# Optimization experiments

Hardware: AMD Instinct MI355X
Metric: run time of the kernel (lower is better)

## Reference

```python
import jax, jax.numpy as jnp
import numpy as np

NUM_HEADS = 12
NUM_BN = 4
HIDDEN = 768
HEAD_DIM = HIDDEN // NUM_HEADS  # 64
SCALE = HEAD_DIM ** -0.5


def setup_inputs() -> dict:
    key = jax.random.key(0)
    k0, k1, k2, k3 = jax.random.split(key, 4)
    B, S = 8, 8192
    x = jax.random.normal(k0, (B, S, HIDDEN), dtype=jnp.float32)
    w_kv = jax.random.normal(k1, (2 * HIDDEN, HIDDEN), dtype=jnp.float32) * 0.02
    w_q = jax.random.normal(k2, (HIDDEN, HIDDEN), dtype=jnp.float32) * 0.02
    w_out = jax.random.normal(k3, (HIDDEN, HIDDEN), dtype=jnp.float32) * 0.02
    b_out = jnp.zeros((HIDDEN,), dtype=jnp.float32)
    return {"x": x, "w_kv": w_kv, "w_q": w_q, "w_out": w_out, "b_out": b_out}


def reference(x, w_kv, w_q, w_out, b_out):
    B, S, H = x.shape
    # kv projection over all tokens: [B, S, 2H] -> split (kv, heads, head_dim)
    kv = (x @ w_kv.T).reshape(B, S, 2, NUM_HEADS, HEAD_DIM)
    k = jnp.transpose(kv[:, :, 0], (0, 2, 1, 3))  # [B, h, S, d]
    v = jnp.transpose(kv[:, :, 1], (0, 2, 1, 3))  # [B, h, S, d]
    # q projection over first NUM_BN tokens only: [B, h, NUM_BN, d]
    q = (x[:, :NUM_BN] @ w_q.T).reshape(B, NUM_BN, NUM_HEADS, HEAD_DIM)
    q = jnp.transpose(q, (0, 2, 1, 3))
    # attention: [B, h, NUM_BN, S]
    att = jax.nn.softmax(jnp.einsum("bhxd,bhyd->bhxy", q, k) * SCALE, axis=-1)
    out = jnp.einsum("bhxy,bhyd->bhxd", att, v)  # [B, h, NUM_BN, d]
    out = jnp.transpose(out, (0, 2, 1, 3)).reshape(B, NUM_BN, H)
    return out @ w_out.T + b_out
```

## Files before the change

### kernel.cpp

```cpp
#include <hip/hip_runtime.h>

typedef unsigned short u16;
typedef __attribute__((ext_vector_type(8))) short short8;
typedef __attribute__((ext_vector_type(4))) float f32x4;
typedef __attribute__((ext_vector_type(8))) __bf16 bf16x8;

__device__ __forceinline__ float b2f(u16 u) {
  unsigned int i = ((unsigned int)u) << 16;
  return __builtin_bit_cast(float, i);
}
__device__ __forceinline__ u16 f2b(float f) {
  unsigned int i = __builtin_bit_cast(unsigned int, f);
  i += 0x7fffu + ((i >> 16) & 1u);
  return (u16)(i >> 16);
}

__global__ __launch_bounds__(256) void cvt_bf16(const float* __restrict__ in,
                                                u16* __restrict__ out, int n8) {
  int i = blockIdx.x * 256 + threadIdx.x;
  if (i >= n8) return;
  f32x4 v0 = *(const f32x4*)(in + (size_t)i * 8);
  f32x4 v1 = *(const f32x4*)(in + (size_t)i * 8 + 4);
  short8 o;
  o[0] = (short)f2b(v0.x); o[1] = (short)f2b(v0.y);
  o[2] = (short)f2b(v0.z); o[3] = (short)f2b(v0.w);
  o[4] = (short)f2b(v1.x); o[5] = (short)f2b(v1.y);
  o[6] = (short)f2b(v1.z); o[7] = (short)f2b(v1.w);
  *(short8*)(out + (size_t)i * 8) = o;
}

__global__ __launch_bounds__(256) void kv_gemm_mfma(const u16* __restrict__ A,
                                                    const u16* __restrict__ B,
                                                    u16* __restrict__ KV, int nb) {
  __shared__ u16 As[128 * 32];
  __shared__ u16 Bs[128 * 32];
  const int tid = threadIdx.x;
  const int lane = tid & 63;
  const int w = tid >> 6;
  const int wr = w >> 1, wc = w & 1;
  const int fr = lane & 15;
  const int fq = lane >> 4;

  const int bid0 = blockIdx.x;
  const int cpx = gridDim.x >> 3;
  const int bid = (bid0 & 7) * cpx + (bid0 >> 3);

  const int nt = bid % 12, mt = bid / 12;
  const int m0 = mt * 128, n0 = nt * 128;

  f32x4 accT[4][4] = {};

  for (int k0 = 0; k0 < 768; k0 += 32) {
#pragma unroll
    for (int i = 0; i < 2; ++i) {
      int c = w * 128 + i * 64 + lane;
      int row = c >> 2, q = c & 3;
      const u16* ga = A + (size_t)(m0 + row) * 768 + k0 + q * 8;
      const u16* gb = B + (size_t)(n0 + row) * 768 + k0 + q * 8;
      __builtin_amdgcn_global_load_lds(
          (const __attribute__((address_space(1))) void*)ga,
          (__attribute__((address_space(3))) void*)(As + (size_t)(w * 128 + i * 64) * 8),
          16, 0, 0);
      __builtin_amdgcn_global_load_lds(
          (const __attribute__((address_space(1))) void*)gb,
          (__attribute__((address_space(3))) void*)(Bs + (size_t)(w * 128 + i * 64) * 8),
          16, 0, 0);
    }
    __syncthreads();

    bf16x8 a[4], b[4];
#pragma unroll
    for (int m = 0; m < 4; ++m)
      a[m] = *(const bf16x8*)(As + (size_t)(wr * 64 + m * 16 + fr) * 32 + fq * 8);
#pragma unroll
    for (int n = 0; n < 4; ++n)
      b[n] = *(const bf16x8*)(Bs + (size_t)(wc * 64 + n * 16 + fr) * 32 + fq * 8);
#pragma unroll
    for (int n = 0; n < 4; ++n)
#pragma unroll
      for (int m = 0; m < 4; ++m)
        accT[n][m] = __builtin_amdgcn_mfma_f32_16x16x32_bf16(b[n], a[m], accT[n][m], 0, 0, 0);
    __syncthreads();
  }

  const int bl = m0 >> 13;
  const int s_ = (m0 & 8191) + wr * 64 + fr;
#pragma unroll
  for (int n = 0; n < 4; ++n) {
    int f0 = n0 + wc * 64 + n * 16 + fq * 4;
    int kvsel = f0 >= 768 ? 1 : 0;
    int h = (f0 >> 6) - kvsel * 12;
    int d0 = f0 & 63;
    u16* outp = KV + ((size_t)(kvsel * nb + bl) * 12 + h) * (8192 * 64) + d0;
#pragma unroll
    for (int m = 0; m < 4; ++m) {
      int s = s_ + m * 16;
      union { u16 q[4]; unsigned long long u; } pk;
      pk.q[0] = f2b(accT[n][m][0]);
      pk.q[1] = f2b(accT[n][m][1]);
      pk.q[2] = f2b(accT[n][m][2]);
      pk.q[3] = f2b(accT[n][m][3]);
      *(unsigned long long*)(outp + (size_t)s * 64) = pk.u;
    }
  }
}

__global__ __launch_bounds__(256) void q_proj(const float* __restrict__ X,
                                              const float* __restrict__ Wq,
                                              float* __restrict__ Q) {
  __shared__ float xs[768];
  const int bid = blockIdx.x;
  const int rrow = bid / 3, cg = bid % 3;
  const int b = rrow >> 2, s = rrow & 3;
  const float* xrow = X + ((size_t)b * 8192 + s) * 768;
  const int t = threadIdx.x;
  if (t < 192) *(f32x4*)&xs[t * 4] = *(const f32x4*)(xrow + t * 4);
  __syncthreads();
  const int c = cg * 256 + t;
  const float* wrow = Wq + (size_t)c * 768;
  float acc = 0.f;
#pragma unroll 8
  for (int jj = 0; jj < 192; ++jj) {
    f32x4 v = *(const f32x4*)(wrow + jj * 4);
    acc += v.x * xs[jj * 4] + v.y * xs[jj * 4 + 1] + v.z * xs[jj * 4 + 2] +
           v.w * xs[jj * 4 + 3];
  }
  Q[(size_t)rrow * 768 + c] = acc * 0.125f;
}

#define CHUNK 256
#define NSCH 32

__global__ __launch_bounds__(256) void attn_part(const u16* __restrict__ KV,
                                                 const float* __restrict__ Q,
                                                 float* __restrict__ Mp,
                                                 float* __restrict__ Lp,
                                                 float* __restrict__ Op,
                                                 int b0, int nb) {
  __shared__ float qsh[4][64];
  __shared__ float sc[4][CHUNK];
  const int tid = threadIdx.x;
  const int bid = blockIdx.x;
  const int ch = bid % NSCH;
  const int rem = bid / NSCH;
  const int h = rem % 12, bl = rem / 12;
  const int b = b0 + bl;

  qsh[tid >> 6][tid & 63] = Q[(size_t)(b * 4 + (tid >> 6)) * 768 + h * 64 + (tid & 63)];
  __syncthreads();

  const u16* Kb = KV + (size_t)(bl * 12 + h) * (8192 * 64) + (size_t)ch * CHUNK * 64;
  const u16* Vb = KV + (size_t)((nb + bl) * 12 + h) * (8192 * 64) + (size_t)ch * CHUNK * 64;

  const int wv = tid >> 6;
  const int lane = tid & 63;
  const int ys = lane >> 3, dc = lane & 7;

  float qr[4][8];
#pragma unroll
  for (int x = 0; x < 4; ++x) {
    f32x4 lo = *(const f32x4*)&qsh[x][dc * 8];
    f32x4 hi = *(const f32x4*)&qsh[x][dc * 8 + 4];
    qr[x][0] = lo.x; qr[x][1] = lo.y; qr[x][2] = lo.z; qr[x][3] = lo.w;
    qr[x][4] = hi.x; qr[x][5] = hi.y; qr[x][6] = hi.z; qr[x][7] = hi.w;
  }

#pragma unroll
  for (int it = 0; it < 8; ++it) {
    const int y = wv * 64 + it * 8 + ys;
    short8 k8 = *(const short8*)(Kb + (size_t)y * 64 + dc * 8);
    float s0 = 0.f, s1 = 0.f, s2 = 0.f, s3 = 0.f;
#pragma unroll
    for (int e = 0; e < 8; ++e) {
      float kv = b2f((u16)k8[e]);
      s0 += kv * qr[0][e]; s1 += kv * qr[1][e];
      s2 += kv * qr[2][e]; s3 += kv * qr[3][e];
    }
#pragma unroll
    for (int off = 1; off <= 4; off <<= 1) {
      s0 += __shfl_xor(s0, off); s1 += __shfl_xor(s1, off);
      s2 += __shfl_xor(s2, off); s3 += __shfl_xor(s3, off);
    }
    if (dc == 0) {
      sc[0][y] = s0; sc[1][y] = s1; sc[2][y] = s2; sc[3][y] = s3;
    }
  }
  __syncthreads();

  const int g = wv;
  const int pidx = (((bl * 12 + h) * 4 + g) * NSCH) + ch;
  {
    float m4 = fmaxf(fmaxf(sc[g][lane], sc[g][lane + 64]),
                     fmaxf(sc[g][lane + 128], sc[g][lane + 192]));
#pragma unroll
    for (int off = 32; off; off >>= 1) m4 = fmaxf(m4, __shfl_xor(m4, off));
    float ls = 0.f;
#pragma unroll
    for (int i = 0; i < 4; ++i) {
      int y = lane + i * 64;
      float p = __expf(sc[g][y] - m4);
      sc[g][y] = p;
      ls += p;
    }
#pragma unroll
    for (int off = 32; off; off >>= 1) ls += __shfl_xor(ls, off);
    if (lane == 0) { Mp[pidx] = m4; Lp[pidx] = ls; }
  }
  __syncthreads();

  {
    float o8[8] = {0.f, 0.f, 0.f, 0.f, 0.f, 0.f, 0.f, 0.f};
#pragma unroll 4
    for (int y0 = 0; y0 < CHUNK; y0 += 8) {
      float p = sc[g][y0 + ys];
      short8 v8 = *(const short8*)(Vb + (size_t)(y0 + ys) * 64 + dc * 8);
#pragma unroll
      for (int e = 0; e < 8; ++e) o8[e] += p * b2f((u16)v8[e]);
    }
#pragma unroll
    for (int off = 32; off >= 8; off >>= 1)
#pragma unroll
      for (int e = 0; e < 8; ++e) o8[e] += __shfl_xor(o8[e], off);
    if (ys == 0) {
      f32x4 lo, hi;
      lo.x = o8[0]; lo.y = o8[1]; lo.z = o8[2]; lo.w = o8[3];
      hi.x = o8[4]; hi.y = o8[5]; hi.z = o8[6]; hi.w = o8[7];
      *(f32x4*)(Op + (size_t)pidx * 64 + dc * 8) = lo;
      *(f32x4*)(Op + (size_t)pidx * 64 + dc * 8 + 4) = hi;
    }
  }
}

__global__ __launch_bounds__(64) void attn_combine(const float* __restrict__ Mp,
                                                   const float* __restrict__ Lp,
                                                   const float* __restrict__ Op,
                                                   float* __restrict__ Att,
                                                   int b0) {
  const int p = blockIdx.x;
  const int d = threadIdx.x;
  const int x = p & 3;
  const int h = (p >> 2) % 12;
  const int bl = p / 48;

  float M = -__builtin_inff();
#pragma unroll 8
  for (int ch = 0; ch < NSCH; ++ch) M = fmaxf(M, Mp[p * NSCH + ch]);
  float L = 0.f, O = 0.f;
#pragma unroll 8
  for (int ch = 0; ch < NSCH; ++ch) {
    float w = __expf(Mp[p * NSCH + ch] - M);
    L += Lp[p * NSCH + ch] * w;
    O += Op[(size_t)(p * NSCH + ch) * 64 + d] * w;
  }
  Att[(size_t)((b0 + bl) * 4 + x) * 768 + h * 64 + d] = O / L;
}

__global__ __launch_bounds__(256) void out_proj(const float* __restrict__ Att,
                                               const float* __restrict__ Wo,
                                               const float* __restrict__ Bo,
                                               float* __restrict__ Out) {
  __shared__ float xs[768];
  const int bid = blockIdx.x;
  const int rrow = bid / 3, cg = bid % 3;
  const int t = threadIdx.x;
  if (t < 192) *(f32x4*)&xs[t * 4] = *(const f32x4*)(Att + (size_t)rrow * 768 + t * 4);
  __syncthreads();
  const int c = cg * 256 + t;
  const float* wrow = Wo + (size_t)c * 768;
  float acc = 0.f;
#pragma unroll 8
  for (int jj = 0; jj < 192; ++jj) {
    f32x4 v = *(const f32x4*)(wrow + jj * 4);
    acc += v.x * xs[jj * 4] + v.y * xs[jj * 4 + 1] + v.z * xs[jj * 4 + 2] +
           v.w * xs[jj * 4 + 3];
  }
  acc += Bo[c];
  Out[(size_t)rrow * 768 + c] = acc;
}

extern "C" void kernel_launch(void* const* d_in, const int* in_sizes, int n_in,
                              void* d_out, int out_size, void* d_ws, size_t ws_size,
                              hipStream_t stream) {
  const float* X = (const float*)d_in[0];
  const float* Wkv = (const float*)d_in[1];
  const float* Wq = (const float*)d_in[2];
  const float* Wo = (const float*)d_in[3];
  const float* Bo = (const float*)d_in[4];
  float* Out = (float*)d_out;

  char* ws = (char*)d_ws;
  size_t off = 0;
  float* Q = (float*)(ws + off); off += 98304;
  float* Att = (float*)(ws + off); off += 98304;
  float* Mp = (float*)(ws + off); off += 384 * NSCH * 4;
  float* Lp = (float*)(ws + off); off += 384 * NSCH * 4;
  float* Op = (float*)(ws + off); off += (size_t)384 * NSCH * 64 * 4;
  u16* Wbf = (u16*)(ws + off); off += 2359296;
  u16* Xbf = (u16*)(ws + off); off += 100663296ull;
  const size_t tail = off;
  const size_t kvPerBatch = 2ull * 12 * 8192 * 64 * 2;

  int nb = 8;
  while (nb > 1 && tail + (size_t)nb * kvPerBatch > ws_size) nb >>= 1;
  const int groups = 8 / nb;
  u16* KV = (u16*)(ws + tail);

  hipLaunchKernelGGL(cvt_bf16, dim3(576), dim3(256), 0, stream, Wkv, Wbf,
                     1536 * 768 / 8);
  hipLaunchKernelGGL(cvt_bf16, dim3(24576), dim3(256), 0, stream, X, Xbf,
                     8 * 8192 * 768 / 8);
  hipLaunchKernelGGL(q_proj, dim3(96), dim3(256), 0, stream, X, Wq, Q);

  for (int g = 0; g < groups; ++g) {
    const int b0 = g * nb;
    hipLaunchKernelGGL(kv_gemm_mfma, dim3(nb * 768), dim3(256), 0, stream,
                       Xbf + (size_t)b0 * 8192 * 768, Wbf, KV, nb);
    hipLaunchKernelGGL(attn_part, dim3(nb * 12 * NSCH), dim3(256), 0, stream,
                       KV, Q, Mp, Lp, Op, b0, nb);
    hipLaunchKernelGGL(attn_combine, dim3(nb * 48), dim3(64), 0, stream,
                       Mp, Lp, Op, Att, b0);
  }
  hipLaunchKernelGGL(out_proj, dim3(96), dim3(256), 0, stream, Att, Wo, Bo, Out);
}
```

Before: 618.5 us.

## Rewrite KV GEMM as 256x256 tile, 8-wave, double-buffered pipelined MFMA kernel

Replaces the 128x128, 256-thread KV projection GEMM with a 256x256-tile, 512-thread kernel. It stages K=64 slices into double-buffered LDS using XOR-swizzled addresses, interleaves global-to-LDS prefetch of later K tiles with four compute phases, and raises wave priority around the MFMA bursts. The aim is to hide memory latency, avoid LDS bank conflicts and raise arithmetic intensity per block. In exchange it uses 128KB of LDS per block and large accumulator register pressure, and relies on hand-placed waitcnt and barriers that must be exactly right.

```diff
diff --git a/kernel.cpp b/kernel.cpp
--- a/kernel.cpp
+++ b/kernel.cpp
@@ -29,80 +29,130 @@
   *(short8*)(out + (size_t)i * 8) = o;
 }
 
-__global__ __launch_bounds__(256) void kv_gemm_mfma(const u16* __restrict__ A,
-                                                    const u16* __restrict__ B,
-                                                    u16* __restrict__ KV, int nb) {
-  __shared__ u16 As[128 * 32];
-  __shared__ u16 Bs[128 * 32];
+#define NT 12
+
+__global__ __launch_bounds__(512, 2) void kv_gemm_8ph(const u16* __restrict__ A,
+                                                      const u16* __restrict__ B,
+                                                      u16* __restrict__ KV, int nb) {
+  __shared__ alignas(16) u16 lds[2][2][16384];
   const int tid = threadIdx.x;
   const int lane = tid & 63;
   const int w = tid >> 6;
-  const int wr = w >> 1, wc = w & 1;
-  const int fr = lane & 15;
-  const int fq = lane >> 4;
+  const int wm = w >> 2, wn = w & 3;
+  const int fr = lane & 15, fq = lane >> 4;
 
   const int bid0 = blockIdx.x;
   const int cpx = gridDim.x >> 3;
   const int bid = (bid0 & 7) * cpx + (bid0 >> 3);
-
-  const int nt = bid % 12, mt = bid / 12;
-  const int m0 = mt * 128, n0 = nt * 128;
-
-  f32x4 accT[4][4] = {};
-
-  for (int k0 = 0; k0 < 768; k0 += 32) {
-#pragma unroll
-    for (int i = 0; i < 2; ++i) {
-      int c = w * 128 + i * 64 + lane;
-      int row = c >> 2, q = c & 3;
-      const u16* ga = A + (size_t)(m0 + row) * 768 + k0 + q * 8;
-      const u16* gb = B + (size_t)(n0 + row) * 768 + k0 + q * 8;
+  const int nt = bid % 6, mt = bid / 6;
+  const int m0 = mt * 256, n0 = nt * 256;
+
+  auto stage = [&](int buf, int op, int hh, int ktile) {
+    const u16* src = op ? B : A;
+    const int r0 = op ? n0 : m0;
+#pragma unroll
+    for (int r = 0; r < 2; ++r) {
+      int c = (r * 8 + w) * 64 + lane;
+      int row = c >> 3;
+      int kb = ((c & 7) * 16) ^ ((row & 7) << 4);
+      const u16* g = src + (size_t)(r0 + hh * 128 + row) * 768 + ktile * 64 + (kb >> 1);
       __builtin_amdgcn_global_load_lds(
-          (const __attribute__((address_space(1))) void*)ga,
-          (__attribute__((address_space(3))) void*)(As + (size_t)(w * 128 + i * 64) * 8),
+          (const __attribute__((address_space(1))) void*)g,
+          (__attribute__((address_space(3))) void*)(&lds[buf][op][hh * 8192 + (r * 8 + w) * 512]),
           16, 0, 0);
-      __builtin_amdgcn_global_load_lds(
-          (const __attribute__((address_space(1))) void*)gb,
-          (__attribute__((address_space(3))) void*)(Bs + (size_t)(w * 128 + i * 64) * 8),
-          16, 0, 0);
-    }
-    __syncthreads();
-
-    bf16x8 a[4], b[4];
-#pragma unroll
-    for (int m = 0; m < 4; ++m)
-      a[m] = *(const bf16x8*)(As + (size_t)(wr * 64 + m * 16 + fr) * 32 + fq * 8);
-#pragma unroll
-    for (int n = 0; n < 4; ++n)
-      b[n] = *(const bf16x8*)(Bs + (size_t)(wc * 64 + n * 16 + fr) * 32 + fq * 8);
-#pragma unroll
-    for (int n = 0; n < 4; ++n)
+    }
+  };
+
+  f32x4 acc[2][2][4][2] = {};
+
+  stage(0, 0, 0, 0); stage(0, 1, 0, 0);
+  stage(0, 0, 1, 0); stage(0, 1, 1, 0);
+  stage(1, 0, 0, 1); stage(1, 1, 0, 1);
+  asm volatile("s_waitcnt vmcnt(4)" ::: "memory");
+  __builtin_amdgcn_sched_barrier(0);
+  __builtin_amdgcn_s_barrier();
+
+#pragma unroll 1
+  for (int T = 0; T < NT; ++T) {
+    const int buf = T & 1;
+#pragma unroll
+    for (int p = 0; p < 4; ++p) {
+      const int ah = p >> 1, bh = p & 1;
+
+      bf16x8 af[4][2], bfr[2][2];
 #pragma unroll
       for (int m = 0; m < 4; ++m)
-        accT[n][m] = __builtin_amdgcn_mfma_f32_16x16x32_bf16(b[n], a[m], accT[n][m], 0, 0, 0);
-    __syncthreads();
+#pragma unroll
+        for (int ks = 0; ks < 2; ++ks) {
+          int row = wm * 64 + m * 16 + fr;
+          int kb = (ks * 64 + fq * 16) ^ ((fr & 7) << 4);
+          af[m][ks] = *(const bf16x8*)((const char*)&lds[buf][0][0] +
+                                       ah * 16384 + row * 128 + kb);
+        }
+#pragma unroll
+      for (int n = 0; n < 2; ++n)
+#pragma unroll
+        for (int ks = 0; ks < 2; ++ks) {
+          int row = wn * 32 + n * 16 + fr;
+          int kb = (ks * 64 + fq * 16) ^ ((fr & 7) << 4);
+          bfr[n][ks] = *(const bf16x8*)((const char*)&lds[buf][1][0] +
+                                        bh * 16384 + row * 128 + kb);
+        }
+
+      if (p == 0)      { if (T + 1 < NT) stage(buf ^ 1, 0, 1, T + 1); }
+      else if (p == 1) { if (T + 1 < NT) stage(buf ^ 1, 1, 1, T + 1); }
+      else if (p == 2) { if (T + 2 < NT) stage(buf, 0, 0, T + 2); }
+      else             { if (T + 2 < NT) stage(buf, 1, 0, T + 2); }
+
+      __builtin_amdgcn_s_barrier();
+      asm volatile("s_waitcnt lgkmcnt(0)" ::: "memory");
+      __builtin_amdgcn_sched_barrier(0);
+
+      __builtin_amdgcn_s_setprio(1);
+#pragma unroll
+      for (int m = 0; m < 4; ++m)
+#pragma unroll
+        for (int n = 0; n < 2; ++n)
+#pragma unroll
+          for (int ks = 0; ks < 2; ++ks)
+            acc[ah][bh][m][n] = __builtin_amdgcn_mfma_f32_16x16x32_bf16(
+                bfr[n][ks], af[m][ks], acc[ah][bh][m][n], 0, 0, 0);
+      __builtin_amdgcn_s_setprio(0);
+
+      if (p < 3) __builtin_amdgcn_s_barrier();
+    }
+    if (T < NT - 1) {
+      if (T < NT - 2) asm volatile("s_waitcnt vmcnt(4)" ::: "memory");
+      else            asm volatile("s_waitcnt vmcnt(0)" ::: "memory");
+      __builtin_amdgcn_sched_barrier(0);
+      __builtin_amdgcn_s_barrier();
+    }
   }
 
   const int bl = m0 >> 13;
-  const int s_ = (m0 & 8191) + wr * 64 + fr;
-#pragma unroll
-  for (int n = 0; n < 4; ++n) {
-    int f0 = n0 + wc * 64 + n * 16 + fq * 4;
-    int kvsel = f0 >= 768 ? 1 : 0;
-    int h = (f0 >> 6) - kvsel * 12;
-    int d0 = f0 & 63;
-    u16* outp = KV + ((size_t)(kvsel * nb + bl) * 12 + h) * (8192 * 64) + d0;
-#pragma unroll
-    for (int m = 0; m < 4; ++m) {
-      int s = s_ + m * 16;
-      union { u16 q[4]; unsigned long long u; } pk;
-      pk.q[0] = f2b(accT[n][m][0]);
-      pk.q[1] = f2b(accT[n][m][1]);
-      pk.q[2] = f2b(accT[n][m][2]);
-      pk.q[3] = f2b(accT[n][m][3]);
-      *(unsigned long long*)(outp + (size_t)s * 64) = pk.u;
-    }
-  }
+  const int sb = m0 & 8191;
+#pragma unroll
+  for (int bh = 0; bh < 2; ++bh)
+#pragma unroll
+    for (int n = 0; n < 2; ++n) {
+      int f0 = n0 + bh * 128 + wn * 32 + n * 16 + fq * 4;
+      int kvsel = f0 >= 768 ? 1 : 0;
+      int h = (f0 >> 6) - kvsel * 12;
+      int d0 = f0 & 63;
+      u16* outp = KV + ((size_t)(kvsel * nb + bl) * 12 + h) * (8192 * 64) + d0;
+#pragma unroll
+      for (int ah = 0; ah < 2; ++ah)
+#pragma unroll
+        for (int m = 0; m < 4; ++m) {
+          int s = sb + ah * 128 + wm * 64 + m * 16 + fr;
+          union { u16 q[4]; unsigned long long u; } pk;
+          pk.q[0] = f2b(acc[ah][bh][m][n][0]);
+          pk.q[1] = f2b(acc[ah][bh][m][n][1]);
+          pk.q[2] = f2b(acc[ah][bh][m][n][2]);
+          pk.q[3] = f2b(acc[ah][bh][m][n][3]);
+          *(unsigned long long*)(outp + (size_t)s * 64) = pk.u;
+        }
+    }
 }
 
 __global__ __launch_bounds__(256) void q_proj(const float* __restrict__ X,
@@ -313,7 +363,7 @@
 
   for (int g = 0; g < groups; ++g) {
     const int b0 = g * nb;
-    hipLaunchKernelGGL(kv_gemm_mfma, dim3(nb * 768), dim3(256), 0, stream,
+    hipLaunchKernelGGL(kv_gemm_8ph, dim3(nb * 192), dim3(512), 0, stream,
                        Xbf + (size_t)b0 * 8192 * 768, Wbf, KV, nb);
     hipLaunchKernelGGL(attn_part, dim3(nb * 12 * NSCH), dim3(256), 0, stream,
                        KV, Q, Mp, Lp, Op, b0, nb);
```

Result: faster. 590.6 us (-4.5%).
